# Kernel tuning notes

Hardware: AMD Instinct MI355X
Metric: run time of the kernel (lower is better)

The kernel has to match this reference:

```python
import jax, jax.numpy as jnp
import numpy as np

B, L, D, NH = 4, 1500, 512, 8
HD = D // NH
EPS = 1e-8            # F.normalize eps
PEPS = 1.1920929e-07  # torch clamp_probs eps for float32
TEMP = 1.0


def setup_inputs():
    key = jax.random.key(0)
    ks = jax.random.split(key, 12)
    s = 1.0 / np.sqrt(D)
    eye = jnp.eye(D, dtype=jnp.float32)
    return {
        "hidden": jax.random.normal(ks[0], (B, L, D), jnp.float32),
        "lengths": jnp.ones((B,), jnp.float32),
        "u_noise": jax.random.uniform(ks[1], (B, L), jnp.float32),
        "W1": jax.random.normal(ks[2], (D, D), jnp.float32) * s,
        "b1": jnp.zeros((D,), jnp.float32),
        "W2": jax.random.normal(ks[3], (D, D), jnp.float32) * s,
        "b2": jnp.zeros((D,), jnp.float32),
        "Wq": eye + jax.random.normal(ks[4], (D, D), jnp.float32) * 0.01,
        "Wk": eye + jax.random.normal(ks[5], (D, D), jnp.float32) * 0.01,
        "sim_bias": jnp.float32(0.098),
        "learned_query": jax.random.normal(ks[6], (D,), jnp.float32),
        "Wpk": eye + jax.random.normal(ks[7], (D, D), jnp.float32) * 0.01,
        "Wpv": eye + jax.random.normal(ks[8], (D, D), jnp.float32) * 0.01,
        "Wpo": eye + jax.random.normal(ks[9], (D, D), jnp.float32) * 0.01,
        "ln_g": jnp.ones((D,), jnp.float32),
        "ln_b": jnp.zeros((D,), jnp.float32),
    }


def reference(hidden, lengths, u_noise, W1, b1, W2, b2, Wq, Wk, sim_bias,
              learned_query, Wpk, Wpv, Wpo, ln_g, ln_b):
    Bb, Ll, Dd = hidden.shape

    def nrm(x):
        n = jnp.sqrt(jnp.sum(x * x, -1, keepdims=True))
        return x / jnp.maximum(n, EPS)

    def mlp(x):
        return jax.nn.gelu(x @ W1.T + b1, approximate=False) @ W2.T + b2

    # boundary logits from adjacent-frame cosine similarity (dropout = eval identity)
    q_in = nrm(hidden[:, :-1]); q = nrm(mlp(q_in) + q_in) @ Wq.T
    k_in = nrm(hidden[:, 1:]);  k = nrm(mlp(k_in) + k_in) @ Wk.T
    cos = jnp.sum(q * k, -1)                                   # (B, L-1)
    probs = jnp.clip((1.0 - (cos + sim_bias)) * 0.5, 0.0, 1.0)
    probs = jnp.pad(probs, ((0, 0), (0, 1)))                   # (B, L)

    # RelaxedBernoulli rsample with explicit logistic noise
    p = jnp.clip(probs, PEPS, 1.0 - PEPS)
    u = jnp.clip(u_noise, PEPS, 1.0 - PEPS)
    soft = jax.nn.sigmoid((jnp.log(p) - jnp.log1p(-p) + jnp.log(u) - jnp.log1p(-u)) / TEMP)
    hard = (soft > 0.5).astype(hidden.dtype)

    idx = jnp.arange(Ll)
    valid_len = jnp.minimum((lengths * (Ll + 1)).astype(jnp.int32) - 1, Ll)
    trunc = (valid_len < Ll)[:, None]
    zmask = trunc & (idx[None] >= valid_len[:, None])
    omask = trunc & (idx[None] == valid_len[:, None])
    soft = jnp.where(omask, 1.0, jnp.where(zmask, 0.0, soft))
    hard = jnp.where(omask, 1.0, jnp.where(zmask, 0.0, hard))
    hard_b = hard - jax.lax.stop_gradient(soft) + soft         # straight-through
    # emergency boundary for all-zero rows
    no_b = (jnp.sum(hard, 1) == 0)[:, None]
    hard_b = jnp.where(no_b & (idx[None] == jnp.minimum(valid_len, Ll - 1)[:, None]), 1.0, hard_b)

    # segment membership (common()): token l in segment s iff exclusive cumsum == s
    seg = jnp.cumsum(hard_b, 1) - hard_b                       # (B, L)
    lmask = idx[None] < (lengths * Ll).astype(jnp.int32)[:, None]
    seg_mask = (seg[:, :, None] == idx[None, None, :].astype(hidden.dtype)) & lmask[:, :, None]  # (B,L,S)

    # layernorm + K/V projections
    mu = jnp.mean(hidden, -1, keepdims=True)
    hv = hidden - mu
    hn = hv / jnp.sqrt(jnp.mean(hv * hv, -1, keepdims=True) + 1e-5) * ln_g + ln_b
    keys = (hn @ Wpk.T).reshape(Bb, Ll, NH, HD)
    vals = (hn @ Wpv.T).reshape(Bb, Ll, NH, HD)

    # query is shared across segments -> scores only differ via the segment mask
    qh = learned_query.reshape(NH, HD)
    base = jnp.einsum('hd,blhd->bhl', qh, keys) * (HD ** -0.5)  # (B,H,L)
    mask_t = jnp.transpose(seg_mask, (0, 2, 1))[:, None]        # (B,1,S,L)
    sc = jnp.where(mask_t, base[:, :, None, :], -jnp.inf)       # (B,H,S,L)
    aw = jnp.nan_to_num(jax.nn.softmax(sc, axis=-1))            # empty segments -> 0 rows
    pooled = jnp.einsum('bhsl,blhd->bshd', aw, vals).reshape(Bb, Ll, Dd)
    return pooled @ Wpo.T                                       # (B, S=L, D)
```

## Files before the change

kernel.cpp:

```cpp
#include <hip/hip_runtime.h>
#include <math.h>

#define Bz 4
#define Lz 1500
#define Dz 512
#define NHz 8
#define Nz (Bz*Lz)
#define PEPSf 1.1920929e-07f

typedef __bf16 bf16x8 __attribute__((ext_vector_type(8)));
typedef unsigned short u16x8 __attribute__((ext_vector_type(8)));
typedef float f32x4 __attribute__((ext_vector_type(4)));
typedef unsigned short us;

__device__ __forceinline__ us f2bf(float f) {
  unsigned u = __float_as_uint(f);
  return (us)((u + 0x7fffu + ((u >> 16) & 1u)) >> 16);
}
__device__ __forceinline__ float bf2f(us b) {
  return __uint_as_float(((unsigned)b) << 16);
}
__device__ __forceinline__ int ti_idx(int row, int col) {
  return (((row >> 4) * 64 + (col >> 3)) << 7) + ((row & 15) << 3) + (col & 7);
}
__device__ __forceinline__ void st_tiled(us* __restrict__ P, int row, int col, us v) {
  P[ti_idx(row, col)] = v;
}

__device__ __forceinline__ bool decode_blk(int bx, int ncg, int& R, int& cg) {
  int xcd = bx & 7, v = bx >> 3;
  cg = v % ncg;
  R = (v / ncg) * 8 + xcd;
  return R < 94;
}

__global__ __launch_bounds__(256) void k_wconv(
    const float* __restrict__ s0, const float* __restrict__ s1, const float* __restrict__ s2,
    const float* __restrict__ s3,
    const float* __restrict__ Wq, const float* __restrict__ Wk,
    const float* __restrict__ Wpk, const float* __restrict__ lq,
    us* __restrict__ h0, us* __restrict__ h1, us* __restrict__ h2, us* __restrict__ h3,
    us* __restrict__ l0, us* __restrict__ l1,
    us* __restrict__ WkTh, us* __restrict__ WkTl, us* __restrict__ WqTh, us* __restrict__ WqTl,
    float* __restrict__ wqe) {
  const int rt = blockIdx.x, mat = blockIdx.y, t = threadIdx.x;
  if (mat == 8) {
    if (rt < 8) {
      for (int d = t; d < Dz; d += 256) {
        float acc = 0.f;
        for (int e = 0; e < 64; ++e) acc += lq[rt * 64 + e] * Wpk[(size_t)(rt * 64 + e) * Dz + d];
        wqe[rt * Dz + d] = acc;
      }
    }
    return;
  }
  const float* S; us* H; us* L = nullptr; bool tr = false;
  switch (mat) {
    case 0: S = s0; H = h0; L = l0; break;
    case 1: S = s1; H = h1; L = l1; break;
    case 2: S = s2; H = h2; break;
    case 3: S = s3; H = h3; break;
    case 4: S = Wk; H = WkTh; L = WkTl; tr = true; break;
    default: S = Wq; H = WqTh; L = WqTl; tr = true; break;
  }
  for (int e = t; e < 8192; e += 256) {
    int mm = e >> 9, c = e & 511;
    float x = tr ? S[(size_t)c * 512 + (rt * 16 + mm)]
                 : S[(size_t)(rt * 16 + mm) * 512 + c];
    us hb = f2bf(x);
    int off = ((rt * 64 + (c >> 3)) << 7) + (mm << 3) + (c & 7);
    H[off] = hb;
    if (L) L[off] = f2bf(x - bf2f(hb));
  }
}

__global__ __launch_bounds__(256) void k_rowprep(const float* __restrict__ h,
    const float* __restrict__ g, const float* __restrict__ bb,
    const float* __restrict__ wqe,
    us* __restrict__ Uh, us* __restrict__ Ul, us* __restrict__ HNh,
    float* __restrict__ base) {
  const int row = blockIdx.x;
  const int t = threadIdx.x;
  const float* x = h + (size_t)row * Dz;
  float x0 = x[t], x1 = x[t + 256];
  float s = x0 + x1, q = x0 * x0 + x1 * x1;
  #pragma unroll
  for (int o = 32; o > 0; o >>= 1) { s += __shfl_xor(s, o, 64); q += __shfl_xor(q, o, 64); }
  __shared__ float ls[4], lq[4];
  __shared__ float xs[Dz];
  if ((t & 63) == 0) { ls[t >> 6] = s; lq[t >> 6] = q; }
  __syncthreads();
  s = ls[0] + ls[1] + ls[2] + ls[3];
  q = lq[0] + lq[1] + lq[2] + lq[3];
  float un = 1.f / fmaxf(sqrtf(q), 1e-8f);
  float u0 = x0 * un, u1 = x1 * un;
  us hb0 = f2bf(u0), hb1 = f2bf(u1);
  st_tiled(Uh, row, t, hb0);       st_tiled(Ul, row, t, f2bf(u0 - bf2f(hb0)));
  st_tiled(Uh, row, t + 256, hb1); st_tiled(Ul, row, t + 256, f2bf(u1 - bf2f(hb1)));
  float mu = s * (1.f / 512.f);
  float var = fmaxf(q * (1.f / 512.f) - mu * mu, 0.f);
  float r = rsqrtf(var + 1e-5f);
  float hn0 = (x0 - mu) * r * g[t] + bb[t];
  float hn1 = (x1 - mu) * r * g[t + 256] + bb[t + 256];
  st_tiled(HNh, row, t, f2bf(hn0));
  st_tiled(HNh, row, t + 256, f2bf(hn1));
  xs[t] = hn0; xs[t + 256] = hn1;
  __syncthreads();
  const int hh = t >> 5, lane = t & 31;
  float accb = 0.f;
  for (int d = lane; d < Dz; d += 32) accb += xs[d] * wqe[hh * Dz + d];
  #pragma unroll
  for (int o = 16; o > 0; o >>= 1) accb += __shfl_xor(accb, o, 32);
  if (lane == 0) base[(size_t)row * NHz + hh] = accb * 0.125f;
}

template<int SPLIT>
__device__ __forceinline__ void gemm_body(
    const us* __restrict__ Ah, const us* __restrict__ Al,
    const us* __restrict__ Bh, const us* __restrict__ Bl,
    const float* __restrict__ bias,
    const us* __restrict__ addH, const us* __restrict__ addL, int doGelu,
    float* __restrict__ outF, us* __restrict__ outH, us* __restrict__ outL,
    int R, int cg, int colbase, int Nrows) {
  const int t = threadIdx.x, w = t >> 6, l = t & 63;
  const int m = l & 15, q = l >> 4;
  const int rt0 = R * 4;
  const int ct0 = cg * 8 + w * 2;
  const int laneoff = q * 128 + m * 8;
  const int nrtm1 = (Nrows >> 4) - 1;

  const u16x8* pa[4]; const u16x8* pal[4];
  const u16x8* pb[2]; const u16x8* pbl[2];
  #pragma unroll
  for (int i = 0; i < 4; ++i) {
    int rt = min(rt0 + i, nrtm1);
    pa[i] = (const u16x8*)(Ah + (size_t)rt * 8192 + laneoff);
    if (SPLIT == 3) pal[i] = (const u16x8*)(Al + (size_t)rt * 8192 + laneoff);
  }
  #pragma unroll
  for (int j = 0; j < 2; ++j) {
    pb[j] = (const u16x8*)(Bh + (size_t)(ct0 + j) * 8192 + laneoff);
    if (SPLIT == 3) pbl[j] = (const u16x8*)(Bl + (size_t)(ct0 + j) * 8192 + laneoff);
  }

  u16x8 bAh[2][4], bAl[2][4], bBh[2][2], bBl[2][2];
  #pragma unroll
  for (int i = 0; i < 4; ++i) {
    bAh[0][i] = pa[i][0];
    if (SPLIT == 3) bAl[0][i] = pal[i][0];
  }
  #pragma unroll
  for (int j = 0; j < 2; ++j) {
    bBh[0][j] = pb[j][0];
    if (SPLIT == 3) bBl[0][j] = pbl[j][0];
  }

  f32x4 acc[4][2];
  #pragma unroll
  for (int i = 0; i < 4; ++i)
    #pragma unroll
    for (int j = 0; j < 2; ++j) acc[i][j] = (f32x4){0.f, 0.f, 0.f, 0.f};

  #pragma unroll 2
  for (int s = 0; s < 16; ++s) {
    const int cur = s & 1, nxt = cur ^ 1;
    const int sn = (s + 1) & 15;
    #pragma unroll
    for (int i = 0; i < 4; ++i) {
      bAh[nxt][i] = pa[i][sn * 64];
      if (SPLIT == 3) bAl[nxt][i] = pal[i][sn * 64];
    }
    #pragma unroll
    for (int j = 0; j < 2; ++j) {
      bBh[nxt][j] = pb[j][sn * 64];
      if (SPLIT == 3) bBl[nxt][j] = pbl[j][sn * 64];
    }
    #pragma unroll
    for (int i = 0; i < 4; ++i)
      #pragma unroll
      for (int j = 0; j < 2; ++j) {
        bf16x8 a = __builtin_bit_cast(bf16x8, bAh[cur][i]);
        bf16x8 b = __builtin_bit_cast(bf16x8, bBh[cur][j]);
        acc[i][j] = __builtin_amdgcn_mfma_f32_16x16x32_bf16(a, b, acc[i][j], 0, 0, 0);
        if (SPLIT == 3) {
          bf16x8 al_ = __builtin_bit_cast(bf16x8, bAl[cur][i]);
          bf16x8 bl_ = __builtin_bit_cast(bf16x8, bBl[cur][j]);
          acc[i][j] = __builtin_amdgcn_mfma_f32_16x16x32_bf16(a, bl_, acc[i][j], 0, 0, 0);
          acc[i][j] = __builtin_amdgcn_mfma_f32_16x16x32_bf16(al_, b, acc[i][j], 0, 0, 0);
        }
      }
  }

  const int row0 = rt0 * 16;
  #pragma unroll
  for (int i = 0; i < 4; ++i) {
    #pragma unroll
    for (int r = 0; r < 4; ++r) {
      const int grow = row0 + i * 16 + q * 4 + r;
      if (grow >= Nrows) continue;
      #pragma unroll
      for (int j = 0; j < 2; ++j) {
        const int gcol = colbase + (w * 2 + j) * 16 + m;
        float v = acc[i][j][r];
        if (bias)   v += bias[gcol];
        if (addH) {
          int ai = ti_idx(grow, gcol);
          v += bf2f(addH[ai]) + bf2f(addL[ai]);
        }
        if (doGelu) v = 0.5f * v * (1.f + erff(v * 0.70710678118654752f));
        if (outF) outF[(size_t)grow * Dz + gcol] = v;
        if (outH) {
          us hb = f2bf(v);
          st_tiled(outH, grow, gcol, hb);
          if (outL) st_tiled(outL, grow, gcol, f2bf(v - bf2f(hb)));
        }
      }
    }
  }
}

__global__ __launch_bounds__(256, 2) void g_t1_vals_gt(
    const us* Uh, const us* Ul, const us* W1h, const us* W1l, const float* b1, us* T1h, us* T1l,
    const us* HNh, const us* Wpvh, float* VALS,
    const us* WkTh, const us* WkTl, const us* WqTh, const us* WqTl, us* Gth, us* Gtl) {
  if (blockIdx.z == 2) {
    int bx = blockIdx.x;
    if (bx >= 32) return;
    gemm_body<3>(WkTh, WkTl, WqTh, WqTl, nullptr, nullptr, nullptr, 0,
                 nullptr, Gth, Gtl, bx >> 2, bx & 3, (bx & 3) * 128, 512);
    return;
  }
  int R, cg;
  if (!decode_blk(blockIdx.x, 4, R, cg)) return;
  if (blockIdx.z == 0)
    gemm_body<3>(Uh, Ul, W1h, W1l, b1, nullptr, nullptr, 1,
                 nullptr, T1h, T1l, R, cg, cg * 128, Nz);
  else
    gemm_body<1>(HNh, nullptr, Wpvh, nullptr, nullptr, nullptr, nullptr, 0,
                 VALS, nullptr, nullptr, R, cg, cg * 128, Nz);
}

__global__ __launch_bounds__(256, 2) void g_w2(
    const us* T1h, const us* T1l, const us* W2h, const us* W2l, const float* b2,
    const us* Uh, const us* Ul, float* M, us* Mh, us* Ml) {
  int R, cg;
  if (!decode_blk(blockIdx.x, 4, R, cg)) return;
  gemm_body<3>(T1h, T1l, W2h, W2l, b2, Uh, Ul, 0, M, Mh, Ml, R, cg, cg * 128, Nz);
}

__global__ __launch_bounds__(256, 2) void g_p(
    const us* Mh, const us* Ml, const us* Gth, const us* Gtl, float* P) {
  int R, cg;
  if (!decode_blk(blockIdx.x, 4, R, cg)) return;
  gemm_body<3>(Mh, Ml, Gth, Gtl, nullptr, nullptr, nullptr, 0,
               P, nullptr, nullptr, R, cg, cg * 128, Nz);
}

__global__ __launch_bounds__(256, 2) void g_out(
    const us* Ph, const us* Wpoh, float* out) {
  int R, cg;
  if (!decode_blk(blockIdx.x, 4, R, cg)) return;
  gemm_body<1>(Ph, nullptr, Wpoh, nullptr, nullptr, nullptr, nullptr, 0,
               out, nullptr, nullptr, R, cg, cg * 128, Nz);
}

__global__ void k_probs(const float* __restrict__ P, const float* __restrict__ M,
                        const float* __restrict__ simb, float* __restrict__ probs) {
  const int l = blockIdx.x, b = blockIdx.y, t = threadIdx.x;
  if (l == Lz - 1) { if (t == 0) probs[(size_t)b * Lz + l] = 0.f; return; }
  const float* pp = P + ((size_t)b * Lz + l) * Dz;
  const float* m0 = M + ((size_t)b * Lz + l) * Dz;
  const float* m1 = M + ((size_t)b * Lz + l + 1) * Dz;
  float accd = 0.f, q0 = 0.f, q1 = 0.f;
  for (int i = t; i < Dz; i += 64) {
    float a = pp[i], x0 = m0[i], x1 = m1[i];
    accd += a * x1; q0 += x0 * x0; q1 += x1 * x1;
  }
  #pragma unroll
  for (int o = 32; o > 0; o >>= 1) {
    accd += __shfl_xor(accd, o, 64);
    q0 += __shfl_xor(q0, o, 64);
    q1 += __shfl_xor(q1, o, 64);
  }
  if (t == 0) {
    float un0 = 1.f / fmaxf(sqrtf(q0), 1e-8f);
    float un1 = 1.f / fmaxf(sqrtf(q1), 1e-8f);
    float cosv = accd * un0 * un1;
    float p = (1.f - (cosv + simb[0])) * 0.5f;
    probs[(size_t)b * Lz + l] = fminf(fmaxf(p, 0.f), 1.f);
  }
}

__global__ __launch_bounds__(256) void k_boundary(const float* __restrict__ probs,
    const float* __restrict__ un, const float* __restrict__ lengths,
    int* __restrict__ seg_start, int* __restrict__ seg_meta) {
  const int b = blockIdx.x, t = threadIdx.x;
  __shared__ float hard[Lz];
  __shared__ float ps[256];
  __shared__ float ws4[4];
  const float len = lengths[b];
  const int valid_len = min((int)(len * (Lz + 1)) - 1, Lz);
  const int Lm = (int)(len * Lz);
  const bool trunc = valid_len < Lz;
  for (int l = t; l < Lz; l += 256) {
    float p = probs[(size_t)b * Lz + l];
    p = fminf(fmaxf(p, PEPSf), 1.f - PEPSf);
    float u = un[(size_t)b * Lz + l];
    u = fminf(fmaxf(u, PEPSf), 1.f - PEPSf);
    float z = logf(p) - log1pf(-p) + logf(u) - log1pf(-u);
    float soft = 1.f / (1.f + expf(-z));
    float hd = soft > 0.5f ? 1.f : 0.f;
    if (trunc && l >= valid_len) hd = (l == valid_len) ? 1.f : 0.f;
    hard[l] = hd;
  }
  __syncthreads();
  float sm = 0.f;
  for (int l = t; l < Lz; l += 256) sm += hard[l];
  #pragma unroll
  for (int o = 32; o > 0; o >>= 1) sm += __shfl_xor(sm, o, 64);
  if ((t & 63) == 0) ws4[t >> 6] = sm;
  __syncthreads();
  float total = ws4[0] + ws4[1] + ws4[2] + ws4[3];
  if (total == 0.f && t == 0) hard[min(valid_len, Lz - 1)] = 1.f;
  __syncthreads();
  const int l0 = t * 6;
  float loc = 0.f;
  for (int i = 0; i < 6; ++i) { int l = l0 + i; if (l < Lz) loc += hard[l]; }
  ps[t] = loc;
  __syncthreads();
  for (int off = 1; off < 256; off <<= 1) {
    float v = (t >= off) ? ps[t - off] : 0.f;
    __syncthreads();
    ps[t] += v;
    __syncthreads();
  }
  float run = ps[t] - loc;
  for (int i = 0; i < 6; ++i) {
    int l = l0 + i; if (l >= Lz) break;
    int seg = (int)(run + 0.5f);
    if (l == 0) seg_start[b * (Lz + 1) + 0] = 0;
    else if (hard[l - 1] > 0.5f) seg_start[b * (Lz + 1) + seg] = l;
    if (l == Lz - 1) {
      int nseg = seg + 1;
      seg_meta[b * 2 + 0] = nseg;
      seg_meta[b * 2 + 1] = Lm;
      seg_start[b * (Lz + 1) + nseg] = Lz;
    }
    run += hard[l];
  }
}

__global__ __launch_bounds__(256) void k_pool(const float* __restrict__ base,
    const float* __restrict__ VALS, const int* __restrict__ seg_start,
    const int* __restrict__ seg_meta, us* __restrict__ Ph) {
  const int s = blockIdx.x, b = blockIdx.y, t = threadIdx.x;
  const int orow = b * Lz + s;
  const int nseg = seg_meta[b * 2], Lm = seg_meta[b * 2 + 1];
  int start = 0, end = 0;
  bool empty = true;
  if (s < nseg) {
    start = seg_start[b * (Lz + 1) + s];
    end = min(seg_start[b * (Lz + 1) + s + 1], Lm);
    empty = start >= end;
  }
  if (empty) { st_tiled(Ph, orow, t, 0); st_tiled(Ph, orow, t + 256, 0); return; }
  const int h = t >> 5, lane = t & 31;
  const float* bp = base + (size_t)b * Lz * NHz + h;
  float m = -1e30f;
  for (int l = start + lane; l < end; l += 32) m = fmaxf(m, bp[(size_t)l * NHz]);
  #pragma unroll
  for (int o = 16; o > 0; o >>= 1) m = fmaxf(m, __shfl_xor(m, o, 32));
  float den = 0.f;
  for (int l = start + lane; l < end; l += 32) den += expf(bp[(size_t)l * NHz] - m);
  #pragma unroll
  for (int o = 16; o > 0; o >>= 1) den += __shfl_xor(den, o, 32);
  float a0 = 0.f, a1 = 0.f;
  const float* vp = VALS + (size_t)b * Lz * Dz + h * 64 + lane;
  for (int l = start; l < end; ++l) {
    float wgt = expf(bp[(size_t)l * NHz] - m);
    a0 += wgt * vp[(size_t)l * Dz];
    a1 += wgt * vp[(size_t)l * Dz + 32];
  }
  float inv = 1.f / den;
  st_tiled(Ph, orow, h * 64 + lane, f2bf(a0 * inv));
  st_tiled(Ph, orow, h * 64 + lane + 32, f2bf(a1 * inv));
}

extern "C" void kernel_launch(void* const* d_in, const int* in_sizes, int n_in,
                              void* d_out, int out_size, void* d_ws, size_t ws_size,
                              hipStream_t stream) {
  const float* hidden  = (const float*)d_in[0];
  const float* lengths = (const float*)d_in[1];
  const float* unoise  = (const float*)d_in[2];
  const float* W1  = (const float*)d_in[3];
  const float* b1  = (const float*)d_in[4];
  const float* W2  = (const float*)d_in[5];
  const float* b2  = (const float*)d_in[6];
  const float* Wq  = (const float*)d_in[7];
  const float* Wk  = (const float*)d_in[8];
  const float* simb   = (const float*)d_in[9];
  const float* lquery = (const float*)d_in[10];
  const float* Wpk = (const float*)d_in[11];
  const float* Wpv = (const float*)d_in[12];
  const float* Wpo = (const float*)d_in[13];
  const float* lng = (const float*)d_in[14];
  const float* lnb = (const float*)d_in[15];
  float* out = (float*)d_out;

  char* p = (char*)d_ws;
  const size_t SF = (size_t)Nz * Dz * 4;
  const size_t TP = (size_t)376 * 8192 * 2;
  const size_t WP = (size_t)32 * 8192 * 2;
  float* M    = (float*)p; p += SF;
  float* PF   = (float*)p; p += SF;
  float* VALS = (float*)p; p += SF;
  us* Uh  = (us*)p; p += TP;
  us* Ul  = (us*)p; p += TP;
  us* T1h = (us*)p; p += TP;
  us* T1l = (us*)p; p += TP;
  us* Mh  = (us*)p; p += TP;
  us* Ml  = (us*)p; p += TP;
  us* HNh = (us*)p; p += TP;
  us* Ph  = (us*)p; p += TP;
  us* W1h = (us*)p; p += WP;
  us* W1l = (us*)p; p += WP;
  us* W2h = (us*)p; p += WP;
  us* W2l = (us*)p; p += WP;
  us* Wpvh = (us*)p; p += WP;
  us* Wpoh = (us*)p; p += WP;
  us* WkTh = (us*)p; p += WP;
  us* WkTl = (us*)p; p += WP;
  us* WqTh = (us*)p; p += WP;
  us* WqTl = (us*)p; p += WP;
  us* Gth  = (us*)p; p += WP;
  us* Gtl  = (us*)p; p += WP;
  float* probs  = (float*)p; p += 24064;
  float* base   = (float*)p; p += 192000;
  int* segst    = (int*)p;   p += 24064;
  int* segmeta  = (int*)p;   p += 256;
  float* wqe    = (float*)p;

  const int G4 = 8 * 12 * 4;

  k_wconv<<<dim3(32, 9), 256, 0, stream>>>(W1, W2, Wpv, Wpo, Wq, Wk, Wpk, lquery,
      W1h, W2h, Wpvh, Wpoh, W1l, W2l, WkTh, WkTl, WqTh, WqTl, wqe);
  k_rowprep<<<Nz, 256, 0, stream>>>(hidden, lng, lnb, wqe, Uh, Ul, HNh, base);
  g_t1_vals_gt<<<dim3(G4, 1, 3), 256, 0, stream>>>(Uh, Ul, W1h, W1l, b1, T1h, T1l,
      HNh, Wpvh, VALS, WkTh, WkTl, WqTh, WqTl, Gth, Gtl);
  g_w2<<<G4, 256, 0, stream>>>(T1h, T1l, W2h, W2l, b2, Uh, Ul, M, Mh, Ml);
  g_p<<<G4, 256, 0, stream>>>(Mh, Ml, Gth, Gtl, PF);
  k_probs<<<dim3(Lz, Bz), 64, 0, stream>>>(PF, M, simb, probs);
  k_boundary<<<Bz, 256, 0, stream>>>(probs, unoise, lengths, segst, segmeta);
  k_pool<<<dim3(Lz, Bz), 256, 0, stream>>>(base, VALS, segst, segmeta, Ph);
  g_out<<<G4, 256, 0, stream>>>(Ph, Wpoh, out);
}
```

Baseline: 243.9 us.

## Fuse norm and dot reductions into GEMM epilogues, drop fp32 intermediates

Removes the k_probs kernel by computing squared row norms in the W2 GEMM epilogue and adjacent-row dot products in the P GEMM epilogue, both accumulated with atomics. This avoids writing and rereading the fp32 M and P matrices. VALS is now stored as bf16 row-major, halving pool read traffic at some precision cost. The GEMM main loop also moves from double to triple buffering with full unroll, which raises register pressure.

```diff
diff --git a/kernel.cpp b/kernel.cpp
--- a/kernel.cpp
+++ b/kernel.cpp
@@ -78,9 +78,10 @@
     const float* __restrict__ g, const float* __restrict__ bb,
     const float* __restrict__ wqe,
     us* __restrict__ Uh, us* __restrict__ Ul, us* __restrict__ HNh,
-    float* __restrict__ base) {
+    float* __restrict__ base, float* __restrict__ qn, float* __restrict__ dot) {
   const int row = blockIdx.x;
   const int t = threadIdx.x;
+  if (t == 0) { qn[row] = 0.f; dot[row] = 0.f; }
   const float* x = h + (size_t)row * Dz;
   float x0 = x[t], x1 = x[t + 256];
   float s = x0 + x1, q = x0 * x0 + x1 * x1;
@@ -120,7 +121,10 @@
     const us* __restrict__ Bh, const us* __restrict__ Bl,
     const float* __restrict__ bias,
     const us* __restrict__ addH, const us* __restrict__ addL, int doGelu,
-    float* __restrict__ outF, us* __restrict__ outH, us* __restrict__ outL,
+    float* __restrict__ outF, us* __restrict__ outR,
+    us* __restrict__ outH, us* __restrict__ outL,
+    float* __restrict__ qnAcc,
+    const us* __restrict__ nxH, const us* __restrict__ nxL, float* __restrict__ dotAcc,
     int R, int cg, int colbase, int Nrows) {
   const int t = threadIdx.x, w = t >> 6, l = t & 63;
   const int m = l & 15, q = l >> 4;
@@ -143,16 +147,19 @@
     if (SPLIT == 3) pbl[j] = (const u16x8*)(Bl + (size_t)(ct0 + j) * 8192 + laneoff);
   }
 
-  u16x8 bAh[2][4], bAl[2][4], bBh[2][2], bBl[2][2];
-  #pragma unroll
-  for (int i = 0; i < 4; ++i) {
-    bAh[0][i] = pa[i][0];
-    if (SPLIT == 3) bAl[0][i] = pal[i][0];
-  }
-  #pragma unroll
-  for (int j = 0; j < 2; ++j) {
-    bBh[0][j] = pb[j][0];
-    if (SPLIT == 3) bBl[0][j] = pbl[j][0];
+  u16x8 bAh[3][4], bAl[3][4], bBh[3][2], bBl[3][2];
+  #pragma unroll
+  for (int pre = 0; pre < 2; ++pre) {
+    #pragma unroll
+    for (int i = 0; i < 4; ++i) {
+      bAh[pre][i] = pa[i][pre * 64];
+      if (SPLIT == 3) bAl[pre][i] = pal[i][pre * 64];
+    }
+    #pragma unroll
+    for (int j = 0; j < 2; ++j) {
+      bBh[pre][j] = pb[j][pre * 64];
+      if (SPLIT == 3) bBl[pre][j] = pbl[j][pre * 64];
+    }
   }
 
   f32x4 acc[4][2];
@@ -161,30 +168,31 @@
     #pragma unroll
     for (int j = 0; j < 2; ++j) acc[i][j] = (f32x4){0.f, 0.f, 0.f, 0.f};
 
-  #pragma unroll 2
+  #pragma unroll
   for (int s = 0; s < 16; ++s) {
-    const int cur = s & 1, nxt = cur ^ 1;
-    const int sn = (s + 1) & 15;
+    const int nb = (s + 2) % 3;
+    const int cb = s % 3;
+    const int sn = (s + 2) & 15;
     #pragma unroll
     for (int i = 0; i < 4; ++i) {
-      bAh[nxt][i] = pa[i][sn * 64];
-      if (SPLIT == 3) bAl[nxt][i] = pal[i][sn * 64];
+      bAh[nb][i] = pa[i][sn * 64];
+      if (SPLIT == 3) bAl[nb][i] = pal[i][sn * 64];
     }
     #pragma unroll
     for (int j = 0; j < 2; ++j) {
-      bBh[nxt][j] = pb[j][sn * 64];
-      if (SPLIT == 3) bBl[nxt][j] = pbl[j][sn * 64];
+      bBh[nb][j] = pb[j][sn * 64];
+      if (SPLIT == 3) bBl[nb][j] = pbl[j][sn * 64];
     }
     #pragma unroll
     for (int i = 0; i < 4; ++i)
       #pragma unroll
       for (int j = 0; j < 2; ++j) {
-        bf16x8 a = __builtin_bit_cast(bf16x8, bAh[cur][i]);
-        bf16x8 b = __builtin_bit_cast(bf16x8, bBh[cur][j]);
+        bf16x8 a = __builtin_bit_cast(bf16x8, bAh[cb][i]);
+        bf16x8 b = __builtin_bit_cast(bf16x8, bBh[cb][j]);
         acc[i][j] = __builtin_amdgcn_mfma_f32_16x16x32_bf16(a, b, acc[i][j], 0, 0, 0);
         if (SPLIT == 3) {
-          bf16x8 al_ = __builtin_bit_cast(bf16x8, bAl[cur][i]);
-          bf16x8 bl_ = __builtin_bit_cast(bf16x8, bBl[cur][j]);
+          bf16x8 al_ = __builtin_bit_cast(bf16x8, bAl[cb][i]);
+          bf16x8 bl_ = __builtin_bit_cast(bf16x8, bBl[cb][j]);
           acc[i][j] = __builtin_amdgcn_mfma_f32_16x16x32_bf16(a, bl_, acc[i][j], 0, 0, 0);
           acc[i][j] = __builtin_amdgcn_mfma_f32_16x16x32_bf16(al_, b, acc[i][j], 0, 0, 0);
         }
@@ -198,6 +206,7 @@
     for (int r = 0; r < 4; ++r) {
       const int grow = row0 + i * 16 + q * 4 + r;
       if (grow >= Nrows) continue;
+      float vv[2];
       #pragma unroll
       for (int j = 0; j < 2; ++j) {
         const int gcol = colbase + (w * 2 + j) * 16 + m;
@@ -208,52 +217,78 @@
           v += bf2f(addH[ai]) + bf2f(addL[ai]);
         }
         if (doGelu) v = 0.5f * v * (1.f + erff(v * 0.70710678118654752f));
+        vv[j] = v;
         if (outF) outF[(size_t)grow * Dz + gcol] = v;
+        if (outR) outR[(size_t)grow * Dz + gcol] = f2bf(v);
         if (outH) {
           us hb = f2bf(v);
           st_tiled(outH, grow, gcol, hb);
           if (outL) st_tiled(outL, grow, gcol, f2bf(v - bf2f(hb)));
         }
       }
+      if (qnAcc) {
+        float part = vv[0] * vv[0] + vv[1] * vv[1];
+        #pragma unroll
+        for (int o = 1; o < 16; o <<= 1) part += __shfl_xor(part, o, 64);
+        if (m == 0) atomicAdd(&qnAcc[grow], part);
+      }
+      if (dotAcc && (grow + 1) < Nrows) {
+        float part = 0.f;
+        #pragma unroll
+        for (int j = 0; j < 2; ++j) {
+          const int gcol = colbase + (w * 2 + j) * 16 + m;
+          int ai = ti_idx(grow + 1, gcol);
+          part += vv[j] * (bf2f(nxH[ai]) + bf2f(nxL[ai]));
+        }
+        #pragma unroll
+        for (int o = 1; o < 16; o <<= 1) part += __shfl_xor(part, o, 64);
+        if (m == 0) atomicAdd(&dotAcc[grow], part);
+      }
     }
   }
 }
 
 __global__ __launch_bounds__(256, 2) void g_t1_vals_gt(
     const us* Uh, const us* Ul, const us* W1h, const us* W1l, const float* b1, us* T1h, us* T1l,
-    const us* HNh, const us* Wpvh, float* VALS,
+    const us* HNh, const us* Wpvh, us* VALSb,
     const us* WkTh, const us* WkTl, const us* WqTh, const us* WqTl, us* Gth, us* Gtl) {
   if (blockIdx.z == 2) {
     int bx = blockIdx.x;
     if (bx >= 32) return;
     gemm_body<3>(WkTh, WkTl, WqTh, WqTl, nullptr, nullptr, nullptr, 0,
-                 nullptr, Gth, Gtl, bx >> 2, bx & 3, (bx & 3) * 128, 512);
+                 nullptr, nullptr, Gth, Gtl, nullptr, nullptr, nullptr, nullptr,
+                 bx >> 2, bx & 3, (bx & 3) * 128, 512);
     return;
   }
   int R, cg;
   if (!decode_blk(blockIdx.x, 4, R, cg)) return;
   if (blockIdx.z == 0)
     gemm_body<3>(Uh, Ul, W1h, W1l, b1, nullptr, nullptr, 1,
-                 nullptr, T1h, T1l, R, cg, cg * 128, Nz);
+                 nullptr, nullptr, T1h, T1l, nullptr, nullptr, nullptr, nullptr,
+                 R, cg, cg * 128, Nz);
   else
     gemm_body<1>(HNh, nullptr, Wpvh, nullptr, nullptr, nullptr, nullptr, 0,
-                 VALS, nullptr, nullptr, R, cg, cg * 128, Nz);
+                 nullptr, VALSb, nullptr, nullptr, nullptr, nullptr, nullptr, nullptr,
+                 R, cg, cg * 128, Nz);
 }
 
 __global__ __launch_bounds__(256, 2) void g_w2(
     const us* T1h, const us* T1l, const us* W2h, const us* W2l, const float* b2,
-    const us* Uh, const us* Ul, float* M, us* Mh, us* Ml) {
+    const us* Uh, const us* Ul, us* Mh, us* Ml, float* qn) {
   int R, cg;
   if (!decode_blk(blockIdx.x, 4, R, cg)) return;
-  gemm_body<3>(T1h, T1l, W2h, W2l, b2, Uh, Ul, 0, M, Mh, Ml, R, cg, cg * 128, Nz);
+  gemm_body<3>(T1h, T1l, W2h, W2l, b2, Uh, Ul, 0,
+               nullptr, nullptr, Mh, Ml, qn, nullptr, nullptr, nullptr,
+               R, cg, cg * 128, Nz);
 }
 
 __global__ __launch_bounds__(256, 2) void g_p(
-    const us* Mh, const us* Ml, const us* Gth, const us* Gtl, float* P) {
+    const us* Mh, const us* Ml, const us* Gth, const us* Gtl, float* dot) {
   int R, cg;
   if (!decode_blk(blockIdx.x, 4, R, cg)) return;
   gemm_body<3>(Mh, Ml, Gth, Gtl, nullptr, nullptr, nullptr, 0,
-               P, nullptr, nullptr, R, cg, cg * 128, Nz);
+               nullptr, nullptr, nullptr, nullptr, nullptr, Mh, Ml, dot,
+               R, cg, cg * 128, Nz);
 }
 
 __global__ __launch_bounds__(256, 2) void g_out(
@@ -261,37 +296,12 @@
   int R, cg;
   if (!decode_blk(blockIdx.x, 4, R, cg)) return;
   gemm_body<1>(Ph, nullptr, Wpoh, nullptr, nullptr, nullptr, nullptr, 0,
-               out, nullptr, nullptr, R, cg, cg * 128, Nz);
-}
-
-__global__ void k_probs(const float* __restrict__ P, const float* __restrict__ M,
-                        const float* __restrict__ simb, float* __restrict__ probs) {
-  const int l = blockIdx.x, b = blockIdx.y, t = threadIdx.x;
-  if (l == Lz - 1) { if (t == 0) probs[(size_t)b * Lz + l] = 0.f; return; }
-  const float* pp = P + ((size_t)b * Lz + l) * Dz;
-  const float* m0 = M + ((size_t)b * Lz + l) * Dz;
-  const float* m1 = M + ((size_t)b * Lz + l + 1) * Dz;
-  float accd = 0.f, q0 = 0.f, q1 = 0.f;
-  for (int i = t; i < Dz; i += 64) {
-    float a = pp[i], x0 = m0[i], x1 = m1[i];
-    accd += a * x1; q0 += x0 * x0; q1 += x1 * x1;
-  }
-  #pragma unroll
-  for (int o = 32; o > 0; o >>= 1) {
-    accd += __shfl_xor(accd, o, 64);
-    q0 += __shfl_xor(q0, o, 64);
-    q1 += __shfl_xor(q1, o, 64);
-  }
-  if (t == 0) {
-    float un0 = 1.f / fmaxf(sqrtf(q0), 1e-8f);
-    float un1 = 1.f / fmaxf(sqrtf(q1), 1e-8f);
-    float cosv = accd * un0 * un1;
-    float p = (1.f - (cosv + simb[0])) * 0.5f;
-    probs[(size_t)b * Lz + l] = fminf(fmaxf(p, 0.f), 1.f);
-  }
-}
-
-__global__ __launch_bounds__(256) void k_boundary(const float* __restrict__ probs,
+               out, nullptr, nullptr, nullptr, nullptr, nullptr, nullptr, nullptr,
+               R, cg, cg * 128, Nz);
+}
+
+__global__ __launch_bounds__(256) void k_boundary(const float* __restrict__ dot,
+    const float* __restrict__ qn, const float* __restrict__ simb,
     const float* __restrict__ un, const float* __restrict__ lengths,
     int* __restrict__ seg_start, int* __restrict__ seg_meta) {
   const int b = blockIdx.x, t = threadIdx.x;
@@ -302,9 +312,17 @@
   const int valid_len = min((int)(len * (Lz + 1)) - 1, Lz);
   const int Lm = (int)(len * Lz);
   const bool trunc = valid_len < Lz;
+  const float sb = simb[0];
   for (int l = t; l < Lz; l += 256) {
-    float p = probs[(size_t)b * Lz + l];
-    p = fminf(fmaxf(p, PEPSf), 1.f - PEPSf);
+    float pr = 0.f;
+    if (l != Lz - 1) {
+      const int row = b * Lz + l;
+      float un0 = 1.f / fmaxf(sqrtf(qn[row]), 1e-8f);
+      float un1 = 1.f / fmaxf(sqrtf(qn[row + 1]), 1e-8f);
+      float cosv = dot[row] * un0 * un1;
+      pr = fminf(fmaxf((1.f - (cosv + sb)) * 0.5f, 0.f), 1.f);
+    }
+    float p = fminf(fmaxf(pr, PEPSf), 1.f - PEPSf);
     float u = un[(size_t)b * Lz + l];
     u = fminf(fmaxf(u, PEPSf), 1.f - PEPSf);
     float z = logf(p) - log1pf(-p) + logf(u) - log1pf(-u);
@@ -351,7 +369,7 @@
 }
 
 __global__ __launch_bounds__(256) void k_pool(const float* __restrict__ base,
-    const float* __restrict__ VALS, const int* __restrict__ seg_start,
+    const us* __restrict__ VALSb, const int* __restrict__ seg_start,
     const int* __restrict__ seg_meta, us* __restrict__ Ph) {
   const int s = blockIdx.x, b = blockIdx.y, t = threadIdx.x;
   const int orow = b * Lz + s;
@@ -375,11 +393,11 @@
   #pragma unroll
   for (int o = 16; o > 0; o >>= 1) den += __shfl_xor(den, o, 32);
   float a0 = 0.f, a1 = 0.f;
-  const float* vp = VALS + (size_t)b * Lz * Dz + h * 64 + lane;
+  const us* vp = VALSb + (size_t)b * Lz * Dz + h * 64 + lane;
   for (int l = start; l < end; ++l) {
     float wgt = expf(bp[(size_t)l * NHz] - m);
-    a0 += wgt * vp[(size_t)l * Dz];
-    a1 += wgt * vp[(size_t)l * Dz + 32];
+    a0 += wgt * bf2f(vp[(size_t)l * Dz]);
+    a1 += wgt * bf2f(vp[(size_t)l * Dz + 32]);
   }
   float inv = 1.f / den;
   st_tiled(Ph, orow, h * 64 + lane, f2bf(a0 * inv));
@@ -408,12 +426,8 @@
   float* out = (float*)d_out;
 
   char* p = (char*)d_ws;
-  const size_t SF = (size_t)Nz * Dz * 4;
   const size_t TP = (size_t)376 * 8192 * 2;
   const size_t WP = (size_t)32 * 8192 * 2;
-  float* M    = (float*)p; p += SF;
-  float* PF   = (float*)p; p += SF;
-  float* VALS = (float*)p; p += SF;
   us* Uh  = (us*)p; p += TP;
   us* Ul  = (us*)p; p += TP;
   us* T1h = (us*)p; p += TP;
@@ -422,6 +436,7 @@
   us* Ml  = (us*)p; p += TP;
   us* HNh = (us*)p; p += TP;
   us* Ph  = (us*)p; p += TP;
+  us* VALSb = (us*)p; p += TP;
   us* W1h = (us*)p; p += WP;
   us* W1l = (us*)p; p += WP;
   us* W2h = (us*)p; p += WP;
@@ -434,7 +449,8 @@
   us* WqTl = (us*)p; p += WP;
   us* Gth  = (us*)p; p += WP;
   us* Gtl  = (us*)p; p += WP;
-  float* probs  = (float*)p; p += 24064;
+  float* dot    = (float*)p; p += 24064;
+  float* qn     = (float*)p; p += 24064;
   float* base   = (float*)p; p += 192000;
   int* segst    = (int*)p;   p += 24064;
   int* segmeta  = (int*)p;   p += 256;
@@ -444,13 +460,12 @@
 
   k_wconv<<<dim3(32, 9), 256, 0, stream>>>(W1, W2, Wpv, Wpo, Wq, Wk, Wpk, lquery,
       W1h, W2h, Wpvh, Wpoh, W1l, W2l, WkTh, WkTl, WqTh, WqTl, wqe);
-  k_rowprep<<<Nz, 256, 0, stream>>>(hidden, lng, lnb, wqe, Uh, Ul, HNh, base);
+  k_rowprep<<<Nz, 256, 0, stream>>>(hidden, lng, lnb, wqe, Uh, Ul, HNh, base, qn, dot);
   g_t1_vals_gt<<<dim3(G4, 1, 3), 256, 0, stream>>>(Uh, Ul, W1h, W1l, b1, T1h, T1l,
-      HNh, Wpvh, VALS, WkTh, WkTl, WqTh, WqTl, Gth, Gtl);
-  g_w2<<<G4, 256, 0, stream>>>(T1h, T1l, W2h, W2l, b2, Uh, Ul, M, Mh, Ml);
-  g_p<<<G4, 256, 0, stream>>>(Mh, Ml, Gth, Gtl, PF);
-  k_probs<<<dim3(Lz, Bz), 64, 0, stream>>>(PF, M, simb, probs);
-  k_boundary<<<Bz, 256, 0, stream>>>(probs, unoise, lengths, segst, segmeta);
-  k_pool<<<dim3(Lz, Bz), 256, 0, stream>>>(base, VALS, segst, segmeta, Ph);
+      HNh, Wpvh, VALSb, WkTh, WkTl, WqTh, WqTl, Gth, Gtl);
+  g_w2<<<G4, 256, 0, stream>>>(T1h, T1l, W2h, W2l, b2, Uh, Ul, Mh, Ml, qn);
+  g_p<<<G4, 256, 0, stream>>>(Mh, Ml, Gth, Gtl, dot);
+  k_boundary<<<Bz, 256, 0, stream>>>(dot, qn, simb, unoise, lengths, segst, segmeta);
+  k_pool<<<dim3(Lz, Bz), 256, 0, stream>>>(base, VALSb, segst, segmeta, Ph);
   g_out<<<G4, 256, 0, stream>>>(Ph, Wpoh, out);
 }
```

Result: slower. 312.7 us (+28.2%).
